# Kernel optimization log

Measured on AMD Instinct MI355X. Metric: run time of the kernel, lower is better.

The kernel has to match this reference:

```python
import jax, jax.numpy as jnp
import numpy as np

H = 2048      # hidden_size
NH = 16       # num_attention_heads
HD = H // NH  # head_dim = 128
B, S = 2, 2048
ROPE_BASE = 10000.0


def setup_inputs() -> dict:
    key = jax.random.key(0)
    ks = jax.random.split(key, 9)
    init = 0.02
    inp = {
        "hidden_states": jax.random.normal(ks[0], (B, S, H), dtype=jnp.float32),
        # torch nn.Linear weights are [out_features, in_features]
        "wq": jax.random.normal(ks[1], (H, H), dtype=jnp.float32) * init,
        "bq": jnp.zeros((H,), dtype=jnp.float32),
        "wk": jax.random.normal(ks[2], (H, H), dtype=jnp.float32) * init,
        "bk": jnp.zeros((H,), dtype=jnp.float32),
        "wv": jax.random.normal(ks[3], (H, H), dtype=jnp.float32) * init,
        "bv": jnp.zeros((H,), dtype=jnp.float32),
        "wo": jax.random.normal(ks[4], (H, H), dtype=jnp.float32) * init,
        "bo": jnp.zeros((H,), dtype=jnp.float32),
    }
    return inp


def _rope_cos_sin(seq_len, dim, dtype):
    # standard RoPE tables: [seq_len, dim]
    inv_freq = 1.0 / (ROPE_BASE ** (jnp.arange(0, dim, 2, dtype=jnp.float32) / dim))
    freqs = jnp.arange(seq_len, dtype=jnp.float32)[:, None] * inv_freq[None, :]
    emb = jnp.concatenate([freqs, freqs], axis=-1)  # [S, dim]
    return jnp.cos(emb).astype(dtype), jnp.sin(emb).astype(dtype)


def _rotate_half(x):
    half = x.shape[-1] // 2
    return jnp.concatenate([-x[..., half:], x[..., :half]], axis=-1)


def reference(hidden_states, wq, bq, wk, bk, wv, bv, wo, bo):
    b, s, h = hidden_states.shape
    scale = HD ** -0.5

    def proj(x, w, bias):
        y = jnp.einsum("bsh,oh->bso", x, w) + bias
        # -> [b, nh, s, hd]
        return y.reshape(b, s, NH, HD).transpose(0, 2, 1, 3)

    q = proj(hidden_states, wq, bq)
    k = proj(hidden_states, wk, bk)
    v = proj(hidden_states, wv, bv)

    # rotary embeddings on q, k
    cos, sin = _rope_cos_sin(s, HD, q.dtype)  # [s, hd]
    q = q * cos + _rotate_half(q) * sin
    k = k * cos + _rotate_half(k) * sin

    # causal additive mask [s, s]
    mask = jnp.triu(jnp.full((s, s), -1e9, dtype=q.dtype), k=1)

    scores = jnp.einsum("bhqd,bhkd->bhqk", q, k) * scale + mask
    probs = jax.nn.softmax(scores, axis=-1)
    attn = jnp.einsum("bhqk,bhkd->bhqd", probs, v)
    attn = attn.transpose(0, 2, 1, 3).reshape(b, s, h)
    out = jnp.einsum("bsh,oh->bso", attn, wo) + bo
    return out
```

## Files before the change

### kernel.cpp

```cpp
#include <hip/hip_runtime.h>

typedef unsigned short u16;
typedef __attribute__((ext_vector_type(8))) __bf16 bf16x8;
typedef __attribute__((ext_vector_type(4))) float f32x4;
typedef __attribute__((ext_vector_type(4))) u16 u16x4;
typedef __attribute__((ext_vector_type(8))) u16 u16x8;

constexpr int S = 2048;
constexpr int H = 2048;
constexpr int NH = 16;
constexpr int HD = 128;
constexpr int M = 4096;
constexpr float SCALE = 0.08838834764831845f;

__device__ __forceinline__ u16 f2bf(float f) {
  union { float f; unsigned u; } v; v.f = f;
  unsigned r = v.u + 0x7fffu + ((v.u >> 16) & 1u);
  return (u16)(r >> 16);
}
__device__ __forceinline__ float bf2f(u16 u) {
  union { unsigned u; float f; } v; v.u = ((unsigned)u) << 16;
  return v.f;
}
__device__ __forceinline__ unsigned cvt_pk_bf16(float lo, float hi) {
  unsigned r;
  asm("v_cvt_pk_bf16_f32 %0, %1, %2" : "=v"(r) : "v"(lo), "v"(hi));
  return r;
}
__device__ __forceinline__ f32x4 MFMA16(bf16x8 a, bf16x8 b, f32x4 c) {
  return __builtin_amdgcn_mfma_f32_16x16x32_bf16(a, b, c, 0, 0, 0);
}

__device__ __forceinline__ void gld16(const u16* g, u16* l) {
  __builtin_amdgcn_global_load_lds(
      (const __attribute__((address_space(1))) void*)g,
      (__attribute__((address_space(3))) void*)l, 16, 0, 0);
}

#define BAR  __builtin_amdgcn_s_barrier()

__global__ __launch_bounds__(256) void cast_kernel(const float* __restrict__ in,
                                                   u16* __restrict__ out, int n) {
  int i = (blockIdx.x * 256 + threadIdx.x) * 4;
  if (i >= n) return;
  float4 v = *(const float4*)(in + i);
  u16x4 o;
  o[0] = f2bf(v.x); o[1] = f2bf(v.y); o[2] = f2bf(v.z); o[3] = f2bf(v.w);
  *(u16x4*)(out + i) = o;
}

__global__ __launch_bounds__(256) void cast4_kernel(const float* __restrict__ i0,
                                                    const float* __restrict__ i1,
                                                    const float* __restrict__ i2,
                                                    const float* __restrict__ i3,
                                                    u16* o0, u16* o1, u16* o2, u16* o3) {
  const float* in; u16* out;
  switch (blockIdx.y) {
    case 0: in = i0; out = o0; break;
    case 1: in = i1; out = o1; break;
    case 2: in = i2; out = o2; break;
    default: in = i3; out = o3; break;
  }
  int i = (blockIdx.x * 256 + threadIdx.x) * 4;
  float4 v = *(const float4*)(in + i);
  u16x4 o;
  o[0] = f2bf(v.x); o[1] = f2bf(v.y); o[2] = f2bf(v.z); o[3] = f2bf(v.w);
  *(u16x4*)(out + i) = o;
}

__global__ __launch_bounds__(256) void concat_bias_k(const float* __restrict__ bq,
                                                     const float* __restrict__ bk,
                                                     const float* __restrict__ bv,
                                                     float* __restrict__ bqkv) {
  int i = blockIdx.x * 256 + threadIdx.x;
  const float* src = (i < 2048) ? bq : (i < 4096) ? bk : bv;
  bqkv[i] = src[i & 2047];
}

__global__ __launch_bounds__(256) void rope_table_k(float* __restrict__ tab) {
  int i = blockIdx.x * 256 + threadIdx.x;
  if (i >= S * 64) return;
  int s = i >> 6, d = i & 63;
  float freq = expf(-(float)d * (9.210340371976184f / 64.f));
  float ang = (float)s * freq;
  tab[i * 2]     = cosf(ang);
  tab[i * 2 + 1] = sinf(ang);
}

template<int EMODE>
__device__ __forceinline__ void gemm128(const u16* __restrict__ A,
                                        const u16* __restrict__ Bw,
                                        const float* __restrict__ bias,
                                        const float* __restrict__ tab,
                                        void* __restrict__ out0, void* __restrict__ out1,
                                        void* __restrict__ out2,
                                        int brow, int bcol,
                                        u16* AsL, u16* BsL) {
  const int t = threadIdx.x;
  const int w = t >> 6, l = t & 63;
  const int wr = w >> 1, wc = w & 1;
  const int lr = l & 15, lg = l >> 4;
  const int swz = lr & 7;

  f32x4 acc[4][4] = {};

  const int sr = t >> 3, sj = t & 7;

  auto STAGE = [&](int BUF, int TILE) {
    u16* da = AsL + BUF * (128 * 64);
    const u16* sa = A + (size_t)brow * H + TILE * 64;
    #pragma unroll
    for (int it = 0; it < 4; ++it) {
      int row = it * 32 + sr;
      gld16(sa + (size_t)row * H + ((sj ^ (row & 7)) * 8), da + (it * 256 + t) * 8);
    }
    u16* db = BsL + BUF * (128 * 64);
    const u16* sb = Bw + (size_t)bcol * H + TILE * 64;
    #pragma unroll
    for (int it = 0; it < 4; ++it) {
      int row = it * 32 + sr;
      gld16(sb + (size_t)row * H + ((sj ^ (row & 7)) * 8), db + (it * 256 + t) * 8);
    }
  };
  auto LDA = [&](int BUF, int KH, bf16x8* aa) {
    const u16* base = AsL + BUF * (128 * 64) + (wr * 64 + lr) * 64;
    #pragma unroll
    for (int i = 0; i < 4; ++i)
      aa[i] = *(const bf16x8*)(base + i * (16 * 64) + (((KH * 4 + lg) ^ swz) * 8));
  };
  auto LDB = [&](int BUF, int KH, bf16x8* bb) {
    const u16* base = BsL + BUF * (128 * 64) + (wc * 64 + lr) * 64;
    #pragma unroll
    for (int n = 0; n < 4; ++n)
      bb[n] = *(const bf16x8*)(base + n * (16 * 64) + (((KH * 4 + lg) ^ swz) * 8));
  };
  auto MM = [&](bf16x8* aa, bf16x8* bb) {
    __builtin_amdgcn_s_setprio(1);
    #pragma unroll
    for (int i = 0; i < 4; ++i)
      #pragma unroll
      for (int n = 0; n < 4; ++n)
        acc[i][n] = MFMA16(aa[i], bb[n], acc[i][n]);
    __builtin_amdgcn_s_setprio(0);
  };

  STAGE(0, 0);
  asm volatile("s_waitcnt vmcnt(0)" ::: "memory");
  BAR;

  int c = 0;
  for (int u = 0; u < 32; ++u) {
    if (u < 31) STAGE(c ^ 1, u + 1);
    bf16x8 aa[4], bb[4];
    LDA(c, 0, aa); LDB(c, 0, bb); MM(aa, bb);
    LDA(c, 1, aa); LDB(c, 1, bb); MM(aa, bb);
    asm volatile("s_waitcnt vmcnt(0)" ::: "memory");
    BAR;
    c ^= 1;
  }

  if constexpr (EMODE == 0) {
    float* C = (float*)out0;
    #pragma unroll
    for (int m = 0; m < 4; ++m) {
      const int row0 = brow + wr * 64 + m * 16 + lg * 4;
      #pragma unroll
      for (int n = 0; n < 4; ++n) {
        const int col = bcol + wc * 64 + n * 16 + lr;
        const float bv = bias[col];
        #pragma unroll
        for (int r = 0; r < 4; ++r)
          C[(size_t)(row0 + r) * H + col] = acc[m][n][r] + bv;
      }
    }
  } else {
    const int sel = bcol >> 11;
    if (sel < 2) {
      float* lf = (float*)AsL;
      u16* Cq = sel ? (u16*)out1 : (u16*)out0;
      const float scl = sel ? 1.f : SCALE;
      #pragma unroll
      for (int m = 0; m < 4; ++m) {
        __syncthreads();
        float mine[4][4];
        #pragma unroll
        for (int n = 0; n < 4; ++n) {
          const float bv = bias[bcol + wc * 64 + n * 16 + lr];
          #pragma unroll
          for (int r = 0; r < 4; ++r) {
            mine[n][r] = acc[m][n][r] + bv;
            lf[w * (16 * 66) + (lg * 4 + r) * 66 + n * 16 + lr] = mine[n][r];
          }
        }
        __syncthreads();
        #pragma unroll
        for (int n = 0; n < 4; ++n) {
          const int j = n * 16 + lr;
          const int hcol = (bcol & 2047) + wc * 64 + j;
          #pragma unroll
          for (int r = 0; r < 4; ++r) {
            const int row = brow + wr * 64 + m * 16 + lg * 4 + r;
            const int s = row & (S - 1);
            float pr = lf[(w ^ 1) * (16 * 66) + (lg * 4 + r) * 66 + j];
            float2 cs = ((const float2*)tab)[s * 64 + j];
            float out = wc ? (mine[n][r] * cs.x + pr * cs.y)
                           : (mine[n][r] * cs.x - pr * cs.y);
            Cq[(size_t)row * H + hcol] = f2bf(out * scl);
          }
        }
      }
    } else {
      u16* Vt = (u16*)out2;
      #pragma unroll
      for (int m = 0; m < 4; ++m) {
        const int row0 = brow + wr * 64 + m * 16 + lg * 4;
        #pragma unroll
        for (int n = 0; n < 4; ++n) {
          const int col = (bcol & 2047) + wc * 64 + n * 16 + lr;
          const float bv = bias[bcol + wc * 64 + n * 16 + lr];
          const int hh = col >> 7, d = col & 127;
          const int b = row0 >> 11, s0 = row0 & (S - 1);
          u16x4 pk;
          #pragma unroll
          for (int r = 0; r < 4; ++r) pk[r] = f2bf(acc[m][n][r] + bv);
          *(u16x4*)(Vt + ((size_t)((b * 16 + hh) * 128 + d)) * S + s0) = pk;
        }
      }
    }
  }
}

__global__ __launch_bounds__(256, 2) void gemm_qkv2(const u16* __restrict__ xb,
                                                    const u16* __restrict__ wqkv,
                                                    const float* __restrict__ bqkv,
                                                    const float* __restrict__ tab,
                                                    u16* Qb, u16* Kb, u16* Vt) {
  __shared__ u16 AsL[2 * 128 * 64];
  __shared__ u16 BsL[2 * 128 * 64];
  const int id = blockIdx.x;
  const int xcd = id & 7, sid = id >> 3;
  const int bx = xcd * 6 + (sid % 6);
  const int by = sid / 6;
  gemm128<3>(xb, wqkv, bqkv, tab, Qb, Kb, Vt, by * 128, bx * 128, AsL, BsL);
}

__global__ __launch_bounds__(256, 2) void gemm_o2(const u16* __restrict__ A,
                                                  const u16* __restrict__ W,
                                                  const float* __restrict__ bias,
                                                  float* __restrict__ C) {
  __shared__ u16 AsL[2 * 128 * 64];
  __shared__ u16 BsL[2 * 128 * 64];
  const int id = blockIdx.x;
  const int xcd = id & 7, sid = id >> 3;
  const int bx = xcd * 2 + (sid & 1);
  const int by = sid >> 1;
  gemm128<0>(A, W, bias, nullptr, C, nullptr, nullptr, by * 128, bx * 128, AsL, BsL);
}

__global__ __launch_bounds__(256) void attn_fwd(const u16* __restrict__ Q,
                                                const u16* __restrict__ Kx,
                                                const u16* __restrict__ Vt,
                                                u16* __restrict__ O) {
  const int id = blockIdx.x;
  const int xcd = id & 7, slot = id >> 3;
  const int bh = (slot >> 4) * 8 + xcd;
  const int pid = slot & 15;
  const int b = bh >> 4, h = bh & 15;
  const int t = threadIdx.x, w = t >> 6, l = t & 63;
  const int lr = l & 15, lg = l >> 4;
  const int swz = lr & 7;

  __shared__ u16 Ks[2][64 * 128];
  __shared__ u16 Vs[2][128 * 64];
  __shared__ u16 P_lds[4][16 * 64];
  u16* pw = &P_lds[w][0];

  const u16* kbase = Kx + (size_t)(b * S) * H + h * HD;
  const u16* vbase = Vt + (size_t)bh * HD * S;

  auto stageK = [&](int bf, int k0) {
    #pragma unroll
    for (int it = 0; it < 4; ++it) {
      int c = it * 256 + t;
      int row = c >> 4, j = c & 15;
      gld16(kbase + (size_t)(k0 + row) * H + ((j ^ (row & 7)) * 8), &Ks[bf][0] + c * 8);
    }
  };
  auto stageV = [&](int bf, int k0) {
    #pragma unroll
    for (int it = 0; it < 4; ++it) {
      int c = it * 256 + t;
      int row = c >> 3, j = c & 7;
      gld16(vbase + (size_t)row * S + k0 + ((j ^ (row & 7)) * 8), &Vs[bf][0] + c * 8);
    }
  };

  int cur = 0;
  for (int qi = 0; qi < 2; ++qi) {
    const int qt = qi ? pid : (31 - pid);
    const int q0 = qt * 64 + w * 16;

    bf16x8 qa[4];
    const u16* qbase = Q + (size_t)(b * S + q0 + lr) * H + h * HD;
    #pragma unroll
    for (int ks = 0; ks < 4; ++ks)
      qa[ks] = *(const bf16x8*)(qbase + ks * 32 + lg * 8);

    f32x4 acc[8] = {};
    float mrun[4], lrun[4];
    #pragma unroll
    for (int r = 0; r < 4; ++r) { mrun[r] = -1e30f; lrun[r] = 0.f; }

    __syncthreads();
    stageK(cur, 0);
    stageV(cur, 0);
    __syncthreads();

    for (int kt = 0; kt <= qt; ++kt) {
      if (kt < qt) {
        stageK(cur ^ 1, (kt + 1) * 64);
        stageV(cur ^ 1, (kt + 1) * 64);
      }
      const u16* kl = &Ks[cur][0];
      const u16* vl = &Vs[cur][0];

      f32x4 sc[4] = {};
      __builtin_amdgcn_s_setprio(1);
      #pragma unroll
      for (int ks = 0; ks < 4; ++ks) {
        #pragma unroll
        for (int f = 0; f < 4; ++f) {
          bf16x8 kf = *(const bf16x8*)(kl + (f * 16 + lr) * 128 + (((ks * 4 + lg) ^ swz) * 8));
          sc[f] = __builtin_amdgcn_mfma_f32_16x16x32_bf16(qa[ks], kf, sc[f], 0, 0, 0);
        }
      }
      __builtin_amdgcn_s_setprio(0);
      const bool diag = (kt == qt);
      float p[4][4];
      #pragma unroll
      for (int f = 0; f < 4; ++f)
        #pragma unroll
        for (int r = 0; r < 4; ++r) {
          float v = sc[f][r];
          if (diag && (f * 16 + lr > w * 16 + lg * 4 + r)) v = -1e30f;
          p[f][r] = v;
        }
      float mx[4];
      #pragma unroll
      for (int r = 0; r < 4; ++r) {
        float m0 = fmaxf(fmaxf(p[0][r], p[1][r]), fmaxf(p[2][r], p[3][r]));
        m0 = fmaxf(m0, __shfl_xor(m0, 1));
        m0 = fmaxf(m0, __shfl_xor(m0, 2));
        m0 = fmaxf(m0, __shfl_xor(m0, 4));
        m0 = fmaxf(m0, __shfl_xor(m0, 8));
        mx[r] = m0;
      }
      bool grow = (mx[0] > mrun[0] + 8.f) || (mx[1] > mrun[1] + 8.f) ||
                  (mx[2] > mrun[2] + 8.f) || (mx[3] > mrun[3] + 8.f);
      if (__any(grow)) {
        float resc[4];
        #pragma unroll
        for (int r = 0; r < 4; ++r) {
          float mnew = fmaxf(mrun[r], mx[r]);
          resc[r] = __expf(mrun[r] - mnew);
          mrun[r] = mnew;
          lrun[r] *= resc[r];
        }
        #pragma unroll
        for (int fd = 0; fd < 8; ++fd) {
          f32x4 a = acc[fd];
          a[0] *= resc[0]; a[1] *= resc[1]; a[2] *= resc[2]; a[3] *= resc[3];
          acc[fd] = a;
        }
      }
      #pragma unroll
      for (int r = 0; r < 4; ++r) {
        float sum = 0.f;
        #pragma unroll
        for (int f = 0; f < 4; ++f) {
          float e = __expf(p[f][r] - mrun[r]);
          p[f][r] = e;
          sum += e;
        }
        sum += __shfl_xor(sum, 1);
        sum += __shfl_xor(sum, 2);
        sum += __shfl_xor(sum, 4);
        sum += __shfl_xor(sum, 8);
        lrun[r] += sum;
      }
      {
        const int r0 = lg * 4;
        #pragma unroll
        for (int f = 0; f < 4; ++f) {
          const int col = f * 16 + lr;
          unsigned w01 = cvt_pk_bf16(p[f][0], p[f][1]);
          unsigned w23 = cvt_pk_bf16(p[f][2], p[f][3]);
          pw[(r0 + 0) * 64 + (col ^ (((r0 + 0) & 7) << 3))] = (u16)(w01 & 0xffffu);
          pw[(r0 + 1) * 64 + (col ^ (((r0 + 1) & 7) << 3))] = (u16)(w01 >> 16);
          pw[(r0 + 2) * 64 + (col ^ (((r0 + 2) & 7) << 3))] = (u16)(w23 & 0xffffu);
          pw[(r0 + 3) * 64 + (col ^ (((r0 + 3) & 7) << 3))] = (u16)(w23 >> 16);
        }
      }
      __builtin_amdgcn_s_setprio(1);
      #pragma unroll
      for (int ks = 0; ks < 2; ++ks) {
        int col0 = ks * 32 + lg * 8;
        bf16x8 pa = *(const bf16x8*)(pw + lr * 64 + (col0 ^ (swz << 3)));
        #pragma unroll
        for (int fd = 0; fd < 8; ++fd) {
          bf16x8 vb = *(const bf16x8*)(vl + (fd * 16 + lr) * 64 + (((ks * 4 + lg) ^ swz) * 8));
          acc[fd] = __builtin_amdgcn_mfma_f32_16x16x32_bf16(pa, vb, acc[fd], 0, 0, 0);
        }
      }
      __builtin_amdgcn_s_setprio(0);
      __syncthreads();
      cur ^= 1;
    }

    u16* ob = O + (size_t)(b * S + q0 + lg * 4) * H + h * HD;
    #pragma unroll
    for (int r = 0; r < 4; ++r) {
      float inv = 1.f / lrun[r];
      #pragma unroll
      for (int fd = 0; fd < 8; ++fd)
        ob[(size_t)r * H + fd * 16 + lr] = f2bf(acc[fd][r] * inv);
    }
  }
}

extern "C" void kernel_launch(void* const* d_in, const int* in_sizes, int n_in,
                              void* d_out, int out_size, void* d_ws, size_t ws_size,
                              hipStream_t stream) {
  const float* x  = (const float*)d_in[0];
  const float* wq = (const float*)d_in[1];
  const float* bq = (const float*)d_in[2];
  const float* wk = (const float*)d_in[3];
  const float* bk = (const float*)d_in[4];
  const float* wv = (const float*)d_in[5];
  const float* bv = (const float*)d_in[6];
  const float* wo = (const float*)d_in[7];
  const float* bo = (const float*)d_in[8];

  char* ws = (char*)d_ws;
  u16*   xb    = (u16*)(ws);
  u16*   wqkvb = (u16*)(ws + (16ull << 20));
  u16*   wob   = (u16*)(ws + (40ull << 20));
  u16*   Qb    = (u16*)(ws + (48ull << 20));
  u16*   Kb    = (u16*)(ws + (64ull << 20));
  u16*   Vt    = (u16*)(ws + (80ull << 20));
  u16*   Ob    = (u16*)(ws + (96ull << 20));
  float* tab   = (float*)(ws + (112ull << 20));
  float* bqkv  = (float*)(ws + (113ull << 20));

  cast_kernel<<<M * H / 1024, 256, 0, stream>>>(x, xb, M * H);
  cast4_kernel<<<dim3(H * H / 1024, 4), 256, 0, stream>>>(
      wq, wk, wv, wo, wqkvb, wqkvb + (size_t)H * H, wqkvb + 2ull * H * H, wob);
  rope_table_k<<<(S * 64 + 255) / 256, 256, 0, stream>>>(tab);
  concat_bias_k<<<24, 256, 0, stream>>>(bq, bk, bv, bqkv);

  gemm_qkv2<<<1536, 256, 0, stream>>>(xb, wqkvb, bqkv, tab, Qb, Kb, Vt);

  attn_fwd<<<512, 256, 0, stream>>>(Qb, Kb, Vt, Ob);

  gemm_o2<<<512, 256, 0, stream>>>(Ob, wob, bo, (float*)d_out);
}
```

Baseline: 280.0 us.

## Enlarge QKV projection GEMM tile to 256x256 with 512-thread blocks

Replaces the 128x128 QKV GEMM (1536 blocks of 256 threads) with a dedicated 256x256-tile kernel using 8 waves in a 2x4 layout, each wave computing 128x64. Larger tiles raise arithmetic intensity and cut global/L2 traffic per FLOP. The RoPE epilogue pairs waves wc and wc^1 via the LDS exchange. Trade-offs: 128KB of LDS per block, more accumulator registers, and only 384 blocks, which leaves a partial wave across the CUs.

```diff
diff --git a/kernel.cpp b/kernel.cpp
--- a/kernel.cpp
+++ b/kernel.cpp
@@ -87,15 +87,155 @@
   tab[i * 2 + 1] = sinf(ang);
 }
 
-template<int EMODE>
-__device__ __forceinline__ void gemm128(const u16* __restrict__ A,
-                                        const u16* __restrict__ Bw,
-                                        const float* __restrict__ bias,
-                                        const float* __restrict__ tab,
-                                        void* __restrict__ out0, void* __restrict__ out1,
-                                        void* __restrict__ out2,
-                                        int brow, int bcol,
-                                        u16* AsL, u16* BsL) {
+__global__ __launch_bounds__(512, 2) void gemm_qkv256(const u16* __restrict__ A,
+                                                      const u16* __restrict__ Bw,
+                                                      const float* __restrict__ bias,
+                                                      const float* __restrict__ tab,
+                                                      u16* __restrict__ Qb,
+                                                      u16* __restrict__ Kb,
+                                                      u16* __restrict__ Vt) {
+  __shared__ u16 AsL[2 * 256 * 64];
+  __shared__ u16 BsL[2 * 256 * 64];
+
+  const int id = blockIdx.x;
+  const int xcd = id & 7, sid = id >> 3;
+  const int bx = xcd * 3 + (sid % 3);
+  const int by = sid / 3;
+  const int brow = by * 256, bcol = bx * 256;
+  const int sel = bcol >> 11;
+
+  const int t = threadIdx.x;
+  const int w = t >> 6, l = t & 63;
+  const int wr = w >> 2, wc = w & 3;
+  const int lr = l & 15, lg = l >> 4;
+  const int swz = lr & 7;
+
+  f32x4 acc[8][4] = {};
+
+  const int sr = t >> 3, sj = t & 7;
+
+  auto STAGE = [&](int BUF, int TILE) {
+    u16* da = AsL + BUF * (256 * 64);
+    const u16* sa = A + (size_t)brow * H + TILE * 64;
+    #pragma unroll
+    for (int it = 0; it < 4; ++it) {
+      int row = it * 64 + sr;
+      gld16(sa + (size_t)row * H + ((sj ^ (row & 7)) * 8), da + (it * 512 + t) * 8);
+    }
+    u16* db = BsL + BUF * (256 * 64);
+    const u16* sb = Bw + (size_t)bcol * H + TILE * 64;
+    #pragma unroll
+    for (int it = 0; it < 4; ++it) {
+      int row = it * 64 + sr;
+      gld16(sb + (size_t)row * H + ((sj ^ (row & 7)) * 8), db + (it * 512 + t) * 8);
+    }
+  };
+  auto LDB = [&](int BUF, int KH, bf16x8* bb) {
+    const u16* base = BsL + BUF * (256 * 64) + (wc * 64 + lr) * 64;
+    #pragma unroll
+    for (int n = 0; n < 4; ++n)
+      bb[n] = *(const bf16x8*)(base + n * (16 * 64) + (((KH * 4 + lg) ^ swz) * 8));
+  };
+  auto LDA4 = [&](int BUF, int KH, int MB, bf16x8* aa) {
+    const u16* base = AsL + BUF * (256 * 64) + (wr * 128 + MB * 16 + lr) * 64;
+    #pragma unroll
+    for (int i = 0; i < 4; ++i)
+      aa[i] = *(const bf16x8*)(base + i * (16 * 64) + (((KH * 4 + lg) ^ swz) * 8));
+  };
+  auto MM16 = [&](int MB, bf16x8* aa, bf16x8* bb) {
+    __builtin_amdgcn_s_setprio(1);
+    #pragma unroll
+    for (int i = 0; i < 4; ++i)
+      #pragma unroll
+      for (int n = 0; n < 4; ++n)
+        acc[MB + i][n] = MFMA16(aa[i], bb[n], acc[MB + i][n]);
+    __builtin_amdgcn_s_setprio(0);
+  };
+
+  STAGE(0, 0);
+  asm volatile("s_waitcnt vmcnt(0)" ::: "memory");
+  BAR;
+
+  int c = 0;
+  for (int u = 0; u < 32; ++u) {
+    if (u < 31) STAGE(c ^ 1, u + 1);
+    bf16x8 aa[4], bb[4];
+    LDB(c, 0, bb);
+    LDA4(c, 0, 0, aa); MM16(0, aa, bb);
+    LDA4(c, 0, 4, aa); MM16(4, aa, bb);
+    LDB(c, 1, bb);
+    LDA4(c, 1, 0, aa); MM16(0, aa, bb);
+    LDA4(c, 1, 4, aa); MM16(4, aa, bb);
+    asm volatile("s_waitcnt vmcnt(0)" ::: "memory");
+    BAR;
+    c ^= 1;
+  }
+
+  if (sel < 2) {
+    float* lf = (float*)AsL;
+    u16* Cq = sel ? Kb : Qb;
+    const float scl = sel ? 1.f : SCALE;
+    #pragma unroll
+    for (int m = 0; m < 8; ++m) {
+      __syncthreads();
+      float mine[4][4];
+      #pragma unroll
+      for (int n = 0; n < 4; ++n) {
+        const float bv = bias[bcol + wc * 64 + n * 16 + lr];
+        #pragma unroll
+        for (int r = 0; r < 4; ++r) {
+          mine[n][r] = acc[m][n][r] + bv;
+          lf[w * (16 * 66) + (lg * 4 + r) * 66 + n * 16 + lr] = mine[n][r];
+        }
+      }
+      __syncthreads();
+      #pragma unroll
+      for (int n = 0; n < 4; ++n) {
+        const int j = n * 16 + lr;
+        const int hcol = (bcol & 2047) + wc * 64 + j;
+        #pragma unroll
+        for (int r = 0; r < 4; ++r) {
+          const int row = brow + wr * 128 + m * 16 + lg * 4 + r;
+          const int s = row & (S - 1);
+          float pr = lf[(w ^ 1) * (16 * 66) + (lg * 4 + r) * 66 + j];
+          float2 cs = ((const float2*)tab)[s * 64 + j];
+          float out = (wc & 1) ? (mine[n][r] * cs.x + pr * cs.y)
+                               : (mine[n][r] * cs.x - pr * cs.y);
+          Cq[(size_t)row * H + hcol] = f2bf(out * scl);
+        }
+      }
+    }
+  } else {
+    #pragma unroll
+    for (int m = 0; m < 8; ++m) {
+      const int row0 = brow + wr * 128 + m * 16 + lg * 4;
+      #pragma unroll
+      for (int n = 0; n < 4; ++n) {
+        const int col = (bcol & 2047) + wc * 64 + n * 16 + lr;
+        const float bv = bias[bcol + wc * 64 + n * 16 + lr];
+        const int hh = col >> 7, d = col & 127;
+        const int b = row0 >> 11, s0 = row0 & (S - 1);
+        u16x4 pk;
+        #pragma unroll
+        for (int r = 0; r < 4; ++r) pk[r] = f2bf(acc[m][n][r] + bv);
+        *(u16x4*)(Vt + ((size_t)((b * 16 + hh) * 128 + d)) * S + s0) = pk;
+      }
+    }
+  }
+}
+
+__global__ __launch_bounds__(256, 2) void gemm_o2(const u16* __restrict__ A,
+                                                  const u16* __restrict__ Bw,
+                                                  const float* __restrict__ bias,
+                                                  float* __restrict__ C) {
+  __shared__ u16 AsL[2 * 128 * 64];
+  __shared__ u16 BsL[2 * 128 * 64];
+  const int id = blockIdx.x;
+  const int xcd = id & 7, sid = id >> 3;
+  const int bx = xcd * 2 + (sid & 1);
+  const int by = sid >> 1;
+  const int brow = by * 128, bcol = bx * 128;
+
   const int t = threadIdx.x;
   const int w = t >> 6, l = t & 63;
   const int wr = w >> 1, wc = w & 1;
@@ -103,7 +243,6 @@
   const int swz = lr & 7;
 
   f32x4 acc[4][4] = {};
-
   const int sr = t >> 3, sj = t & 7;
 
   auto STAGE = [&](int BUF, int TILE) {
@@ -159,102 +298,18 @@
     c ^= 1;
   }
 
-  if constexpr (EMODE == 0) {
-    float* C = (float*)out0;
-    #pragma unroll
-    for (int m = 0; m < 4; ++m) {
-      const int row0 = brow + wr * 64 + m * 16 + lg * 4;
-      #pragma unroll
-      for (int n = 0; n < 4; ++n) {
-        const int col = bcol + wc * 64 + n * 16 + lr;
-        const float bv = bias[col];
-        #pragma unroll
-        for (int r = 0; r < 4; ++r)
-          C[(size_t)(row0 + r) * H + col] = acc[m][n][r] + bv;
-      }
-    }
-  } else {
-    const int sel = bcol >> 11;
-    if (sel < 2) {
-      float* lf = (float*)AsL;
-      u16* Cq = sel ? (u16*)out1 : (u16*)out0;
-      const float scl = sel ? 1.f : SCALE;
-      #pragma unroll
-      for (int m = 0; m < 4; ++m) {
-        __syncthreads();
-        float mine[4][4];
-        #pragma unroll
-        for (int n = 0; n < 4; ++n) {
-          const float bv = bias[bcol + wc * 64 + n * 16 + lr];
-          #pragma unroll
-          for (int r = 0; r < 4; ++r) {
-            mine[n][r] = acc[m][n][r] + bv;
-            lf[w * (16 * 66) + (lg * 4 + r) * 66 + n * 16 + lr] = mine[n][r];
-          }
-        }
-        __syncthreads();
-        #pragma unroll
-        for (int n = 0; n < 4; ++n) {
-          const int j = n * 16 + lr;
-          const int hcol = (bcol & 2047) + wc * 64 + j;
-          #pragma unroll
-          for (int r = 0; r < 4; ++r) {
-            const int row = brow + wr * 64 + m * 16 + lg * 4 + r;
-            const int s = row & (S - 1);
-            float pr = lf[(w ^ 1) * (16 * 66) + (lg * 4 + r) * 66 + j];
-            float2 cs = ((const float2*)tab)[s * 64 + j];
-            float out = wc ? (mine[n][r] * cs.x + pr * cs.y)
-                           : (mine[n][r] * cs.x - pr * cs.y);
-            Cq[(size_t)row * H + hcol] = f2bf(out * scl);
-          }
-        }
-      }
-    } else {
-      u16* Vt = (u16*)out2;
-      #pragma unroll
-      for (int m = 0; m < 4; ++m) {
-        const int row0 = brow + wr * 64 + m * 16 + lg * 4;
-        #pragma unroll
-        for (int n = 0; n < 4; ++n) {
-          const int col = (bcol & 2047) + wc * 64 + n * 16 + lr;
-          const float bv = bias[bcol + wc * 64 + n * 16 + lr];
-          const int hh = col >> 7, d = col & 127;
-          const int b = row0 >> 11, s0 = row0 & (S - 1);
-          u16x4 pk;
-          #pragma unroll
-          for (int r = 0; r < 4; ++r) pk[r] = f2bf(acc[m][n][r] + bv);
-          *(u16x4*)(Vt + ((size_t)((b * 16 + hh) * 128 + d)) * S + s0) = pk;
-        }
-      }
+  #pragma unroll
+  for (int m = 0; m < 4; ++m) {
+    const int row0 = brow + wr * 64 + m * 16 + lg * 4;
+    #pragma unroll
+    for (int n = 0; n < 4; ++n) {
+      const int col = bcol + wc * 64 + n * 16 + lr;
+      const float bv = bias[col];
+      #pragma unroll
+      for (int r = 0; r < 4; ++r)
+        C[(size_t)(row0 + r) * H + col] = acc[m][n][r] + bv;
     }
   }
-}
-
-__global__ __launch_bounds__(256, 2) void gemm_qkv2(const u16* __restrict__ xb,
-                                                    const u16* __restrict__ wqkv,
-                                                    const float* __restrict__ bqkv,
-                                                    const float* __restrict__ tab,
-                                                    u16* Qb, u16* Kb, u16* Vt) {
-  __shared__ u16 AsL[2 * 128 * 64];
-  __shared__ u16 BsL[2 * 128 * 64];
-  const int id = blockIdx.x;
-  const int xcd = id & 7, sid = id >> 3;
-  const int bx = xcd * 6 + (sid % 6);
-  const int by = sid / 6;
-  gemm128<3>(xb, wqkv, bqkv, tab, Qb, Kb, Vt, by * 128, bx * 128, AsL, BsL);
-}
-
-__global__ __launch_bounds__(256, 2) void gemm_o2(const u16* __restrict__ A,
-                                                  const u16* __restrict__ W,
-                                                  const float* __restrict__ bias,
-                                                  float* __restrict__ C) {
-  __shared__ u16 AsL[2 * 128 * 64];
-  __shared__ u16 BsL[2 * 128 * 64];
-  const int id = blockIdx.x;
-  const int xcd = id & 7, sid = id >> 3;
-  const int bx = xcd * 2 + (sid & 1);
-  const int by = sid >> 1;
-  gemm128<0>(A, W, bias, nullptr, C, nullptr, nullptr, by * 128, bx * 128, AsL, BsL);
 }
 
 __global__ __launch_bounds__(256) void attn_fwd(const u16* __restrict__ Q,
@@ -458,7 +513,7 @@
   rope_table_k<<<(S * 64 + 255) / 256, 256, 0, stream>>>(tab);
   concat_bias_k<<<24, 256, 0, stream>>>(bq, bk, bv, bqkv);
 
-  gemm_qkv2<<<1536, 256, 0, stream>>>(xb, wqkvb, bqkv, tab, Qb, Kb, Vt);
+  gemm_qkv256<<<384, 512, 0, stream>>>(xb, wqkvb, bqkv, tab, Qb, Kb, Vt);
 
   attn_fwd<<<512, 256, 0, stream>>>(Qb, Kb, Vt, Ob);
 
```

New measurement: 308.9 us. +10.3%, slower.

## Use triple-buffered BK=32 GEMM pipeline and merge prep kernels into one launch

Applied to the files above, without the earlier changes.

The projection GEMMs move from a double-buffered K=64 tile loop to a triple-buffered K=32 loop. Each step waits with vmcnt(4), so one future stage stays in flight while the current tile is computed. Smaller LDS tiles let launch bounds request three blocks per CU, which aims to hide global-load latency better. The four prep kernels (x cast, weight casts, RoPE table, bias concat) are also merged into one launch to cut launch overhead. The cost is more barriers per K and a changed swizzle that must stay correct.

```diff
diff --git a/kernel.cpp b/kernel.cpp
--- a/kernel.cpp
+++ b/kernel.cpp
@@ -39,100 +39,108 @@
 
 #define BAR  __builtin_amdgcn_s_barrier()
 
-__global__ __launch_bounds__(256) void cast_kernel(const float* __restrict__ in,
-                                                   u16* __restrict__ out, int n) {
-  int i = (blockIdx.x * 256 + threadIdx.x) * 4;
-  if (i >= n) return;
-  float4 v = *(const float4*)(in + i);
-  u16x4 o;
-  o[0] = f2bf(v.x); o[1] = f2bf(v.y); o[2] = f2bf(v.z); o[3] = f2bf(v.w);
-  *(u16x4*)(out + i) = o;
-}
-
-__global__ __launch_bounds__(256) void cast4_kernel(const float* __restrict__ i0,
-                                                    const float* __restrict__ i1,
-                                                    const float* __restrict__ i2,
-                                                    const float* __restrict__ i3,
-                                                    u16* o0, u16* o1, u16* o2, u16* o3) {
-  const float* in; u16* out;
-  switch (blockIdx.y) {
-    case 0: in = i0; out = o0; break;
-    case 1: in = i1; out = o1; break;
-    case 2: in = i2; out = o2; break;
-    default: in = i3; out = o3; break;
-  }
-  int i = (blockIdx.x * 256 + threadIdx.x) * 4;
-  float4 v = *(const float4*)(in + i);
-  u16x4 o;
-  o[0] = f2bf(v.x); o[1] = f2bf(v.y); o[2] = f2bf(v.z); o[3] = f2bf(v.w);
-  *(u16x4*)(out + i) = o;
-}
-
-__global__ __launch_bounds__(256) void concat_bias_k(const float* __restrict__ bq,
-                                                     const float* __restrict__ bk,
-                                                     const float* __restrict__ bv,
-                                                     float* __restrict__ bqkv) {
-  int i = blockIdx.x * 256 + threadIdx.x;
+__global__ __launch_bounds__(256) void prep_kernel(const float* __restrict__ x,
+                                                   const float* __restrict__ wq,
+                                                   const float* __restrict__ wk,
+                                                   const float* __restrict__ wv,
+                                                   const float* __restrict__ wo,
+                                                   const float* __restrict__ bq,
+                                                   const float* __restrict__ bk,
+                                                   const float* __restrict__ bv,
+                                                   u16* __restrict__ xb,
+                                                   u16* __restrict__ wqkvb,
+                                                   u16* __restrict__ wob,
+                                                   float* __restrict__ tab,
+                                                   float* __restrict__ bqkv) {
+  const int NX = (M * H) / 1024;
+  const int NW = (H * H) / 1024;
+  int bid = blockIdx.x;
+  if (bid < NX + 4 * NW) {
+    const float* in;
+    u16* out;
+    if (bid < NX) { in = x; out = xb; }
+    else {
+      int z = (bid - NX) / NW;
+      bid = NX + ((bid - NX) % NW);
+      int lb = (blockIdx.x - NX) % NW;
+      switch (z) {
+        case 0: in = wq; out = wqkvb; break;
+        case 1: in = wk; out = wqkvb + (size_t)H * H; break;
+        case 2: in = wv; out = wqkvb + 2ull * H * H; break;
+        default: in = wo; out = wob; break;
+      }
+      int i = (lb * 256 + threadIdx.x) * 4;
+      float4 v = *(const float4*)(in + i);
+      u16x4 o;
+      o[0] = f2bf(v.x); o[1] = f2bf(v.y); o[2] = f2bf(v.z); o[3] = f2bf(v.w);
+      *(u16x4*)(out + i) = o;
+      return;
+    }
+    int i = (bid * 256 + threadIdx.x) * 4;
+    float4 v = *(const float4*)(in + i);
+    u16x4 o;
+    o[0] = f2bf(v.x); o[1] = f2bf(v.y); o[2] = f2bf(v.z); o[3] = f2bf(v.w);
+    *(u16x4*)(out + i) = o;
+    return;
+  }
+  bid -= NX + 4 * NW;
+  if (bid < 512) {
+    int i = bid * 256 + threadIdx.x;
+    int s = i >> 6, d = i & 63;
+    float freq = expf(-(float)d * (9.210340371976184f / 64.f));
+    float ang = (float)s * freq;
+    tab[i * 2]     = cosf(ang);
+    tab[i * 2 + 1] = sinf(ang);
+    return;
+  }
+  bid -= 512;
+  int i = bid * 256 + threadIdx.x;
   const float* src = (i < 2048) ? bq : (i < 4096) ? bk : bv;
   bqkv[i] = src[i & 2047];
 }
 
-__global__ __launch_bounds__(256) void rope_table_k(float* __restrict__ tab) {
-  int i = blockIdx.x * 256 + threadIdx.x;
-  if (i >= S * 64) return;
-  int s = i >> 6, d = i & 63;
-  float freq = expf(-(float)d * (9.210340371976184f / 64.f));
-  float ang = (float)s * freq;
-  tab[i * 2]     = cosf(ang);
-  tab[i * 2 + 1] = sinf(ang);
-}
-
 template<int EMODE>
-__device__ __forceinline__ void gemm128(const u16* __restrict__ A,
-                                        const u16* __restrict__ Bw,
-                                        const float* __restrict__ bias,
-                                        const float* __restrict__ tab,
-                                        void* __restrict__ out0, void* __restrict__ out1,
-                                        void* __restrict__ out2,
-                                        int brow, int bcol,
-                                        u16* AsL, u16* BsL) {
+__device__ __forceinline__ void gemm32(const u16* __restrict__ A,
+                                       const u16* __restrict__ Bw,
+                                       const float* __restrict__ bias,
+                                       const float* __restrict__ tab,
+                                       void* __restrict__ out0, void* __restrict__ out1,
+                                       void* __restrict__ out2,
+                                       int brow, int bcol,
+                                       u16* AsL, u16* BsL) {
   const int t = threadIdx.x;
   const int w = t >> 6, l = t & 63;
   const int wr = w >> 1, wc = w & 1;
   const int lr = l & 15, lg = l >> 4;
-  const int swz = lr & 7;
+  const int swz = (lr >> 1) & 3;
 
   f32x4 acc[4][4] = {};
 
-  const int sr = t >> 3, sj = t & 7;
+  const int c0 = t, c1 = 256 + t;
+  const int r0 = c0 >> 2, j0 = c0 & 3;
+  const int r1 = c1 >> 2, j1 = c1 & 3;
 
   auto STAGE = [&](int BUF, int TILE) {
-    u16* da = AsL + BUF * (128 * 64);
-    const u16* sa = A + (size_t)brow * H + TILE * 64;
-    #pragma unroll
-    for (int it = 0; it < 4; ++it) {
-      int row = it * 32 + sr;
-      gld16(sa + (size_t)row * H + ((sj ^ (row & 7)) * 8), da + (it * 256 + t) * 8);
-    }
-    u16* db = BsL + BUF * (128 * 64);
-    const u16* sb = Bw + (size_t)bcol * H + TILE * 64;
-    #pragma unroll
-    for (int it = 0; it < 4; ++it) {
-      int row = it * 32 + sr;
-      gld16(sb + (size_t)row * H + ((sj ^ (row & 7)) * 8), db + (it * 256 + t) * 8);
-    }
-  };
-  auto LDA = [&](int BUF, int KH, bf16x8* aa) {
-    const u16* base = AsL + BUF * (128 * 64) + (wr * 64 + lr) * 64;
+    u16* da = AsL + BUF * (128 * 32);
+    const u16* sa = A + (size_t)brow * H + TILE * 32;
+    gld16(sa + (size_t)r0 * H + ((j0 ^ ((r0 >> 1) & 3)) * 8), da + c0 * 8);
+    gld16(sa + (size_t)r1 * H + ((j1 ^ ((r1 >> 1) & 3)) * 8), da + c1 * 8);
+    u16* db = BsL + BUF * (128 * 32);
+    const u16* sb = Bw + (size_t)bcol * H + TILE * 32;
+    gld16(sb + (size_t)r0 * H + ((j0 ^ ((r0 >> 1) & 3)) * 8), db + c0 * 8);
+    gld16(sb + (size_t)r1 * H + ((j1 ^ ((r1 >> 1) & 3)) * 8), db + c1 * 8);
+  };
+  auto LDA = [&](int BUF, bf16x8* aa) {
+    const u16* base = AsL + BUF * (128 * 32) + (wr * 64 + lr) * 32;
     #pragma unroll
     for (int i = 0; i < 4; ++i)
-      aa[i] = *(const bf16x8*)(base + i * (16 * 64) + (((KH * 4 + lg) ^ swz) * 8));
-  };
-  auto LDB = [&](int BUF, int KH, bf16x8* bb) {
-    const u16* base = BsL + BUF * (128 * 64) + (wc * 64 + lr) * 64;
+      aa[i] = *(const bf16x8*)(base + i * (16 * 32) + ((lg ^ swz) * 8));
+  };
+  auto LDB = [&](int BUF, bf16x8* bb) {
+    const u16* base = BsL + BUF * (128 * 32) + (wc * 64 + lr) * 32;
     #pragma unroll
     for (int n = 0; n < 4; ++n)
-      bb[n] = *(const bf16x8*)(base + n * (16 * 64) + (((KH * 4 + lg) ^ swz) * 8));
+      bb[n] = *(const bf16x8*)(base + n * (16 * 32) + ((lg ^ swz) * 8));
   };
   auto MM = [&](bf16x8* aa, bf16x8* bb) {
     __builtin_amdgcn_s_setprio(1);
@@ -145,18 +153,30 @@
   };
 
   STAGE(0, 0);
+  STAGE(1, 1);
+
+  int cc = 0, cs = 2;
+  for (int u = 0; u < 62; ++u) {
+    asm volatile("s_waitcnt vmcnt(4)" ::: "memory");
+    BAR;
+    STAGE(cs, u + 2);
+    bf16x8 aa[4], bb[4];
+    LDA(cc, aa); LDB(cc, bb); MM(aa, bb);
+    cc = (cc == 2) ? 0 : cc + 1;
+    cs = (cs == 2) ? 0 : cs + 1;
+  }
+  asm volatile("s_waitcnt vmcnt(4)" ::: "memory");
+  BAR;
+  {
+    bf16x8 aa[4], bb[4];
+    LDA(cc, aa); LDB(cc, bb); MM(aa, bb);
+    cc = (cc == 2) ? 0 : cc + 1;
+  }
   asm volatile("s_waitcnt vmcnt(0)" ::: "memory");
   BAR;
-
-  int c = 0;
-  for (int u = 0; u < 32; ++u) {
-    if (u < 31) STAGE(c ^ 1, u + 1);
+  {
     bf16x8 aa[4], bb[4];
-    LDA(c, 0, aa); LDB(c, 0, bb); MM(aa, bb);
-    LDA(c, 1, aa); LDB(c, 1, bb); MM(aa, bb);
-    asm volatile("s_waitcnt vmcnt(0)" ::: "memory");
-    BAR;
-    c ^= 1;
+    LDA(cc, aa); LDB(cc, bb); MM(aa, bb);
   }
 
   if constexpr (EMODE == 0) {
@@ -202,9 +222,9 @@
             const int row = brow + wr * 64 + m * 16 + lg * 4 + r;
             const int s = row & (S - 1);
             float pr = lf[(w ^ 1) * (16 * 66) + (lg * 4 + r) * 66 + j];
-            float2 cs = ((const float2*)tab)[s * 64 + j];
-            float out = wc ? (mine[n][r] * cs.x + pr * cs.y)
-                           : (mine[n][r] * cs.x - pr * cs.y);
+            float2 cs2 = ((const float2*)tab)[s * 64 + j];
+            float out = wc ? (mine[n][r] * cs2.x + pr * cs2.y)
+                           : (mine[n][r] * cs2.x - pr * cs2.y);
             Cq[(size_t)row * H + hcol] = f2bf(out * scl);
           }
         }
@@ -230,31 +250,31 @@
   }
 }
 
-__global__ __launch_bounds__(256, 2) void gemm_qkv2(const u16* __restrict__ xb,
-                                                    const u16* __restrict__ wqkv,
-                                                    const float* __restrict__ bqkv,
-                                                    const float* __restrict__ tab,
-                                                    u16* Qb, u16* Kb, u16* Vt) {
-  __shared__ u16 AsL[2 * 128 * 64];
-  __shared__ u16 BsL[2 * 128 * 64];
+__global__ __launch_bounds__(256, 3) void gemm_qkv32(const u16* __restrict__ xb,
+                                                     const u16* __restrict__ wqkv,
+                                                     const float* __restrict__ bqkv,
+                                                     const float* __restrict__ tab,
+                                                     u16* Qb, u16* Kb, u16* Vt) {
+  __shared__ u16 AsL[3 * 128 * 32];
+  __shared__ u16 BsL[3 * 128 * 32];
   const int id = blockIdx.x;
   const int xcd = id & 7, sid = id >> 3;
   const int bx = xcd * 6 + (sid % 6);
   const int by = sid / 6;
-  gemm128<3>(xb, wqkv, bqkv, tab, Qb, Kb, Vt, by * 128, bx * 128, AsL, BsL);
-}
-
-__global__ __launch_bounds__(256, 2) void gemm_o2(const u16* __restrict__ A,
-                                                  const u16* __restrict__ W,
-                                                  const float* __restrict__ bias,
-                                                  float* __restrict__ C) {
-  __shared__ u16 AsL[2 * 128 * 64];
-  __shared__ u16 BsL[2 * 128 * 64];
+  gemm32<3>(xb, wqkv, bqkv, tab, Qb, Kb, Vt, by * 128, bx * 128, AsL, BsL);
+}
+
+__global__ __launch_bounds__(256, 3) void gemm_o32(const u16* __restrict__ A,
+                                                   const u16* __restrict__ W,
+                                                   const float* __restrict__ bias,
+                                                   float* __restrict__ C) {
+  __shared__ u16 AsL[3 * 128 * 32];
+  __shared__ u16 BsL[3 * 128 * 32];
   const int id = blockIdx.x;
   const int xcd = id & 7, sid = id >> 3;
   const int bx = xcd * 2 + (sid & 1);
   const int by = sid >> 1;
-  gemm128<0>(A, W, bias, nullptr, C, nullptr, nullptr, by * 128, bx * 128, AsL, BsL);
+  gemm32<0>(A, W, bias, nullptr, C, nullptr, nullptr, by * 128, bx * 128, AsL, BsL);
 }
 
 __global__ __launch_bounds__(256) void attn_fwd(const u16* __restrict__ Q,
@@ -452,15 +472,13 @@
   float* tab   = (float*)(ws + (112ull << 20));
   float* bqkv  = (float*)(ws + (113ull << 20));
 
-  cast_kernel<<<M * H / 1024, 256, 0, stream>>>(x, xb, M * H);
-  cast4_kernel<<<dim3(H * H / 1024, 4), 256, 0, stream>>>(
-      wq, wk, wv, wo, wqkvb, wqkvb + (size_t)H * H, wqkvb + 2ull * H * H, wob);
-  rope_table_k<<<(S * 64 + 255) / 256, 256, 0, stream>>>(tab);
-  concat_bias_k<<<24, 256, 0, stream>>>(bq, bk, bv, bqkv);
-
-  gemm_qkv2<<<1536, 256, 0, stream>>>(xb, wqkvb, bqkv, tab, Qb, Kb, Vt);
+  const int NPREP = (M * H) / 1024 + 4 * (H * H) / 1024 + 512 + 24;
+  prep_kernel<<<NPREP, 256, 0, stream>>>(x, wq, wk, wv, wo, bq, bk, bv,
+                                         xb, wqkvb, wob, tab, bqkv);
+
+  gemm_qkv32<<<1536, 256, 0, stream>>>(xb, wqkvb, bqkv, tab, Qb, Kb, Vt);
 
   attn_fwd<<<512, 256, 0, stream>>>(Qb, Kb, Vt, Ob);
 
-  gemm_o2<<<512, 256, 0, stream>>>(Ob, wob, bo, (float*)d_out);
-}
+  gemm_o32<<<512, 256, 0, stream>>>(Ob, wob, bo, (float*)d_out);
+}
```

Result: slower. 285.7 us (+2.1%).
